# Optimization experiments

Hardware: AMD Instinct MI355X
Metric: run time of the kernel (lower is better)

## Reference

```python
import jax, jax.numpy as jnp
import numpy as np

B, S, D = 4, 2048, 768
H = 12
HD = D // H  # 64

def setup_inputs() -> dict:
    key = jax.random.key(0)
    ks = jax.random.split(key, 5)
    scale = 0.02
    return {
        "x": jax.random.normal(ks[0], (B, S, D), dtype=jnp.float32),
        "w_qkv": jax.random.normal(ks[1], (D, 3 * D), dtype=jnp.float32) * scale,
        "b_qkv": jax.random.normal(ks[2], (3 * D,), dtype=jnp.float32) * scale,
        "w_proj": jax.random.normal(ks[3], (D, D), dtype=jnp.float32) * scale,
        "b_proj": jax.random.normal(ks[4], (D,), dtype=jnp.float32) * scale,
    }

def reference(x, w_qkv, b_qkv, w_proj, b_proj):
    bsz, seq_len, dim = x.shape
    qkv = x @ w_qkv + b_qkv                      # [B,S,3D]
    q, k, v = jnp.split(qkv, 3, axis=-1)
    # [B,S,D] -> [B,H,S,HD]
    def heads(t):
        return t.reshape(bsz, seq_len, H, HD).transpose(0, 2, 1, 3)
    q, k, v = heads(q), heads(k), heads(v)
    scores = jnp.einsum('bhqd,bhkd->bhqk', q, k) * (1.0 / np.sqrt(HD))
    causal = jnp.tril(jnp.ones((seq_len, seq_len), dtype=bool))
    scores = jnp.where(causal[None, None], scores, -jnp.inf)
    attn = jax.nn.softmax(scores.astype(jnp.float32), axis=-1).astype(scores.dtype)
    y = jnp.einsum('bhqk,bhkd->bhqd', attn, v)   # [B,H,S,HD]
    y = y.transpose(0, 2, 1, 3).reshape(bsz, seq_len, dim)
    return y @ w_proj + b_proj
```

## Files before the change

### kernel.cpp

```cpp
#include <hip/hip_runtime.h>
#include <hip/hip_bf16.h>
#include <cstdint>

#define BDIM 768
#define HN 12
#define HDIM 64
#define SEQ 2048
#define BATCH 4
#define MTOT (BATCH * SEQ)

typedef __attribute__((ext_vector_type(8))) short bfrag;
typedef __attribute__((ext_vector_type(4))) float f32x4;

union pfu { bfrag f; unsigned u[4]; };

static __device__ __forceinline__ unsigned short f2bf(float f) {
    union { float f; unsigned u; } v; v.f = f;
    unsigned r = v.u + 0x7FFF + ((v.u >> 16) & 1);
    return (unsigned short)(r >> 16);
}

static __device__ __forceinline__ float fexp2(float x) {
    float r; asm("v_exp_f32 %0, %1" : "=v"(r) : "v"(x)); return r;
}

static __device__ __forceinline__ unsigned cvt_pk_bf16(float lo, float hi) {
    unsigned r;
    asm("v_cvt_pk_bf16_f32 %0, %1, %2" : "=v"(r) : "v"(lo), "v"(hi));
    return r;
}

#if __has_builtin(__builtin_amdgcn_permlane32_swap) && __has_builtin(__builtin_amdgcn_permlane16_swap)
#define HAVE_PERMLANE 1
#else
#define HAVE_PERMLANE 0
#endif

static __device__ __forceinline__ float redmax16(float x) {
#if HAVE_PERMLANE
    union { float f; unsigned u; } a; a.f = x;
    auto r = __builtin_amdgcn_permlane16_swap(a.u, a.u, false, false);
    union { unsigned u; float f; } p, q; p.u = r[0]; q.u = r[1];
    return fmaxf(p.f, q.f);
#else
    return fmaxf(x, __shfl_xor(x, 16));
#endif
}

static __device__ __forceinline__ float redmax32(float x) {
#if HAVE_PERMLANE
    union { float f; unsigned u; } a; a.f = x;
    auto r = __builtin_amdgcn_permlane32_swap(a.u, a.u, false, false);
    union { unsigned u; float f; } p, q; p.u = r[0]; q.u = r[1];
    return fmaxf(p.f, q.f);
#else
    return fmaxf(x, __shfl_xor(x, 32));
#endif
}

__global__ __launch_bounds__(256) void conv_f32_bf16(
    const float* __restrict__ in, unsigned short* __restrict__ out, int n8,
    int* __restrict__ qctr)
{
    if (blockIdx.x == 0 && threadIdx.x < 8) qctr[threadIdx.x] = 0;
    const int i = blockIdx.x * 256 + threadIdx.x;
    if (i >= n8) return;
    const float4 a = ((const float4*)in)[i * 2];
    const float4 b = ((const float4*)in)[i * 2 + 1];
    bfrag o;
    o[0] = f2bf(a.x); o[1] = f2bf(a.y); o[2] = f2bf(a.z); o[3] = f2bf(a.w);
    o[4] = f2bf(b.x); o[5] = f2bf(b.y); o[6] = f2bf(b.z); o[7] = f2bf(b.w);
    ((bfrag*)out)[i] = o;
}

__global__ __launch_bounds__(256) void transpose_f32_bf16(
    const float* __restrict__ in, unsigned short* __restrict__ out, int R, int C)
{
    __shared__ unsigned short t[64][72];
    const int tid = threadIdx.x;
    const int c0 = blockIdx.x * 64, r0 = blockIdx.y * 64;
    #pragma unroll
    for (int i = 0; i < 4; ++i) {
        const int r = (tid >> 4) + i * 16;
        const int c = (tid & 15) * 4;
        const float4 v = *(const float4*)&in[(size_t)(r0 + r) * C + c0 + c];
        t[c + 0][r] = f2bf(v.x);
        t[c + 1][r] = f2bf(v.y);
        t[c + 2][r] = f2bf(v.z);
        t[c + 3][r] = f2bf(v.w);
    }
    __syncthreads();
    #pragma unroll
    for (int i = 0; i < 2; ++i) {
        const int c = (tid >> 3) + i * 32;
        const int r = (tid & 7) * 8;
        *(bfrag*)&out[(size_t)(c0 + c) * R + r0 + r] = *(const bfrag*)&t[c][r];
    }
}

__global__ __launch_bounds__(256) void gemm_qkv(
    const unsigned short* __restrict__ A,
    const unsigned short* __restrict__ Bt,
    const float* __restrict__ bias,
    unsigned short* __restrict__ qb,
    unsigned short* __restrict__ kb,
    unsigned short* __restrict__ vTt)
{
    __shared__ unsigned short As[128 * 64];
    __shared__ unsigned short Bs[128 * 64];

    const int tid  = threadIdx.x;
    const int lane = tid & 63;
    const int wid  = tid >> 6;
    const int l15  = lane & 15;
    const int l4   = lane >> 4;

    const int nwg  = (int)(gridDim.x * gridDim.y);
    const int flat = (int)(blockIdx.y * gridDim.x + blockIdx.x);
    const int swz  = (flat & 7) * (nwg >> 3) + (flat >> 3);
    const int m0 = (swz / (int)gridDim.x) * 128;
    const int n0 = (swz % (int)gridDim.x) * 128;

    const int wm = (wid >> 1) * 64;
    const int wn = (wid & 1) * 64;

    f32x4 acc[4][4] = {};

    for (int k0 = 0; k0 < BDIM; k0 += 64) {
        __syncthreads();
        #pragma unroll
        for (int i = 0; i < 4; ++i) {
            const int row = wid * 32 + i * 8 + (lane >> 3);
            const int ck  = (((lane & 7) ^ (row & 7)) * 8);
            __builtin_amdgcn_global_load_lds(
                (const __attribute__((address_space(1))) void*)(A + (size_t)(m0 + row) * BDIM + k0 + ck),
                (__attribute__((address_space(3))) void*)(As + (wid * 4 + i) * 512),
                16, 0, 0);
            __builtin_amdgcn_global_load_lds(
                (const __attribute__((address_space(1))) void*)(Bt + (size_t)(n0 + row) * BDIM + k0 + ck),
                (__attribute__((address_space(3))) void*)(Bs + (wid * 4 + i) * 512),
                16, 0, 0);
        }
        __syncthreads();

        #pragma unroll
        for (int ks = 0; ks < 2; ++ks) {
            bfrag af[4], bfv[4];
            #pragma unroll
            for (int mi = 0; mi < 4; ++mi) {
                const int row = wm + mi * 16 + l15;
                const int ch  = (ks * 4 + l4) ^ (row & 7);
                af[mi] = *(const bfrag*)(As + row * 64 + ch * 8);
            }
            #pragma unroll
            for (int ni = 0; ni < 4; ++ni) {
                const int row = wn + ni * 16 + l15;
                const int ch  = (ks * 4 + l4) ^ (row & 7);
                bfv[ni] = *(const bfrag*)(Bs + row * 64 + ch * 8);
            }
            #pragma unroll
            for (int mi = 0; mi < 4; ++mi)
                #pragma unroll
                for (int ni = 0; ni < 4; ++ni)
                    acc[mi][ni] = __builtin_amdgcn_mfma_f32_16x16x32_bf16(
                        af[mi], bfv[ni], acc[mi][ni], 0, 0, 0);
        }
    }

    const int nb = n0 + wn;
    if (nb < 1536) {
        unsigned short* dst = (nb < 768) ? qb : kb;
        const int coff = (nb < 768) ? 0 : 768;
        #pragma unroll
        for (int mi = 0; mi < 4; ++mi)
            #pragma unroll
            for (int ni = 0; ni < 4; ++ni) {
                const int n = nb + ni * 16 + l15;
                const float bv = bias[n];
                #pragma unroll
                for (int r = 0; r < 4; ++r) {
                    const int m = m0 + wm + mi * 16 + l4 * 4 + r;
                    dst[(size_t)m * BDIM + (n - coff)] = f2bf(acc[mi][ni][r] + bv);
                }
            }
    } else {
        #pragma unroll
        for (int mi = 0; mi < 4; ++mi)
            #pragma unroll
            for (int ni = 0; ni < 4; ++ni) {
                const int n = nb + ni * 16 + l15;
                const float bv = bias[n];
                const size_t vrow = (size_t)(m0 >> 11) * 768 + (n - 1536);
                const int mbase = m0 + wm + mi * 16 + l4 * 4;
                const int scol = mbase & (SEQ - 1);
                uint2 u2;
                u2.x = (unsigned)f2bf(acc[mi][ni][0] + bv)
                     | ((unsigned)f2bf(acc[mi][ni][1] + bv) << 16);
                u2.y = (unsigned)f2bf(acc[mi][ni][2] + bv)
                     | ((unsigned)f2bf(acc[mi][ni][3] + bv) << 16);
                *(uint2*)(vTt + vrow * SEQ + scol) = u2;
            }
    }
}

__global__ __launch_bounds__(256) void gemm_proj(
    const unsigned short* __restrict__ A,
    const unsigned short* __restrict__ Bt,
    const float* __restrict__ bias,
    float* __restrict__ C)
{
    __shared__ unsigned short As[64 * 64];
    __shared__ unsigned short Bs[128 * 64];

    const int tid  = threadIdx.x;
    const int lane = tid & 63;
    const int wid  = tid >> 6;
    const int l15  = lane & 15;
    const int l4   = lane >> 4;

    const int nwg  = (int)(gridDim.x * gridDim.y);
    const int flat = (int)(blockIdx.y * gridDim.x + blockIdx.x);
    const int swz  = (flat & 7) * (nwg >> 3) + (flat >> 3);
    const int m0 = (swz / (int)gridDim.x) * 64;
    const int n0 = (swz % (int)gridDim.x) * 128;

    const int wm = (wid >> 1) * 32;
    const int wn = (wid & 1) * 64;

    f32x4 acc[2][4] = {};

    for (int k0 = 0; k0 < BDIM; k0 += 64) {
        __syncthreads();
        #pragma unroll
        for (int i = 0; i < 2; ++i) {
            const int row = wid * 16 + i * 8 + (lane >> 3);
            const int ck  = (((lane & 7) ^ (row & 7)) * 8);
            __builtin_amdgcn_global_load_lds(
                (const __attribute__((address_space(1))) void*)(A + (size_t)(m0 + row) * BDIM + k0 + ck),
                (__attribute__((address_space(3))) void*)(As + (wid * 16 + i * 8) * 64),
                16, 0, 0);
        }
        #pragma unroll
        for (int i = 0; i < 4; ++i) {
            const int row = wid * 32 + i * 8 + (lane >> 3);
            const int ck  = (((lane & 7) ^ (row & 7)) * 8);
            __builtin_amdgcn_global_load_lds(
                (const __attribute__((address_space(1))) void*)(Bt + (size_t)(n0 + row) * BDIM + k0 + ck),
                (__attribute__((address_space(3))) void*)(Bs + (wid * 32 + i * 8) * 64),
                16, 0, 0);
        }
        __syncthreads();

        #pragma unroll
        for (int ks = 0; ks < 2; ++ks) {
            bfrag af[2], bfv[4];
            #pragma unroll
            for (int mi = 0; mi < 2; ++mi) {
                const int row = wm + mi * 16 + l15;
                const int ch  = (ks * 4 + l4) ^ (row & 7);
                af[mi] = *(const bfrag*)(As + row * 64 + ch * 8);
            }
            #pragma unroll
            for (int ni = 0; ni < 4; ++ni) {
                const int row = wn + ni * 16 + l15;
                const int ch  = (ks * 4 + l4) ^ (row & 7);
                bfv[ni] = *(const bfrag*)(Bs + row * 64 + ch * 8);
            }
            #pragma unroll
            for (int mi = 0; mi < 2; ++mi)
                #pragma unroll
                for (int ni = 0; ni < 4; ++ni)
                    acc[mi][ni] = __builtin_amdgcn_mfma_f32_16x16x32_bf16(
                        af[mi], bfv[ni], acc[mi][ni], 0, 0, 0);
        }
    }

    #pragma unroll
    for (int mi = 0; mi < 2; ++mi)
        #pragma unroll
        for (int ni = 0; ni < 4; ++ni) {
            const int n = n0 + wn + ni * 16 + l15;
            const float bv = bias[n];
            #pragma unroll
            for (int r = 0; r < 4; ++r) {
                const int m = m0 + wm + mi * 16 + l4 * 4 + r;
                C[(size_t)m * BDIM + n] = acc[mi][ni][r] + bv;
            }
        }
}

#define C2 0.18033688011112042f
#define THR 8.0f

__global__ __launch_bounds__(256, 2) void attn_flash_mfma(
    const unsigned short* __restrict__ qb,
    const unsigned short* __restrict__ kb,
    const unsigned short* __restrict__ vT,
    unsigned short* __restrict__ yatt,
    int* __restrict__ qctr)
{
    __shared__ unsigned short Ks[3][64 * 64];
    __shared__ unsigned short Vs[3][64 * 64];

    const int hint = blockIdx.x & 7;
    const int tid  = threadIdx.x;
    const int lane = tid & 63;
    const int wid  = tid >> 6;
    const int l15  = lane & 15;
    const int l4   = lane >> 4;

    bfrag onesf;
    #pragma unroll
    for (int j = 0; j < 8; ++j) onesf[j] = (short)0x3F80;

    for (;;) {
        __syncthreads();
        if (tid == 0) *(int*)&Ks[0][0] = atomicAdd(&qctr[hint], 1);
        __syncthreads();
        const int it = *(const int*)&Ks[0][0];
        if (it >= 96) break;
        __syncthreads();

        const int bh = hint * 6 + (it % 6);
        const int p  = 15 - (it / 6);
        const int h = bh % HN, b = bh / HN;
        const int q0 = p * 128;
        const int ktmax = 2 * p + 1;

        const unsigned short* kg = kb + (size_t)b * SEQ * BDIM + h * HDIM;
        const unsigned short* vg = vT + (size_t)bh * HDIM * SEQ;

        bfrag qf[2][2];
        {
            const unsigned short* qr0 =
                qb + (size_t)(b * SEQ + q0 + wid * 16 + l15) * BDIM + h * HDIM;
            qf[0][0] = *(const bfrag*)(qr0 + l4 * 8);
            qf[0][1] = *(const bfrag*)(qr0 + 32 + l4 * 8);
            const unsigned short* qr1 = qr0 + (size_t)64 * BDIM;
            qf[1][0] = *(const bfrag*)(qr1 + l4 * 8);
            qf[1][1] = *(const bfrag*)(qr1 + 32 + l4 * 8);
        }

        f32x4 acc0[4] = {}, acc1[4] = {};
        f32x4 accl0 = {}, accl1 = {};
        float m0v = -3.0e38f, m1v = -3.0e38f;

        pfu pf0[2], pf1[2];
        bfrag vr[2][4];
        #pragma unroll
        for (int ks = 0; ks < 2; ++ks) {
            #pragma unroll
            for (int i = 0; i < 4; ++i) { pf0[ks].u[i] = 0u; pf1[ks].u[i] = 0u; }
            #pragma unroll
            for (int ds = 0; ds < 4; ++ds)
                #pragma unroll
                for (int j = 0; j < 8; ++j) vr[ks][ds][j] = 0;
        }

        auto stage = [&](int bufi, int ktile) {
            const int k0 = ktile * 64;
            #pragma unroll
            for (int i = 0; i < 2; ++i) {
                const int row = wid * 16 + i * 8 + (lane >> 3);
                const int ck  = ((lane & 7) ^ (row & 7)) * 8;
                __builtin_amdgcn_global_load_lds(
                    (const __attribute__((address_space(1))) void*)(kg + (size_t)(k0 + row) * BDIM + ck),
                    (__attribute__((address_space(3))) void*)(&Ks[bufi][(wid * 16 + i * 8) * 64]),
                    16, 0, 0);
                __builtin_amdgcn_global_load_lds(
                    (const __attribute__((address_space(1))) void*)(vg + (size_t)row * SEQ + k0 + ck),
                    (__attribute__((address_space(3))) void*)(&Vs[bufi][(wid * 16 + i * 8) * 64]),
                    16, 0, 0);
            }
        };

        auto softmax_dance = [&](f32x4* s, float& mm, pfu* pf, f32x4* acc, f32x4& accl) {
            float mx = s[0][0];
            #pragma unroll
            for (int cs = 0; cs < 4; ++cs)
                #pragma unroll
                for (int r = 0; r < 4; ++r) mx = fmaxf(mx, s[cs][r]);
            mx = redmax16(mx);
            mx = redmax32(mx);
            const float mx2 = mx * C2;

            if (!__all(mx2 <= mm + THR)) {
                const float mnew = fmaxf(mm, mx2);
                const float fac  = fexp2(mm - mnew);
                mm = mnew;
                #pragma unroll
                for (int r = 0; r < 4; ++r) {
                    const float fr = __shfl(fac, (lane & 48) | (l4 * 4 + r));
                    #pragma unroll
                    for (int ds = 0; ds < 4; ++ds) acc[ds][r] *= fr;
                    accl[r] *= fr;
                }
            }

            #pragma unroll
            for (int cs = 0; cs < 4; ++cs)
                #pragma unroll
                for (int r = 0; r < 4; ++r)
                    s[cs][r] = fexp2(fmaf(s[cs][r], C2, -mm));

            unsigned pk[4][2];
            #pragma unroll
            for (int cs = 0; cs < 4; ++cs) {
                pk[cs][0] = cvt_pk_bf16(s[cs][0], s[cs][1]);
                pk[cs][1] = cvt_pk_bf16(s[cs][2], s[cs][3]);
            }
            #pragma unroll
            for (int ks = 0; ks < 2; ++ks)
                #pragma unroll
                for (int i = 0; i < 2; ++i) {
#if HAVE_PERMLANE
                    auto r1 = __builtin_amdgcn_permlane32_swap(
                        pk[ks * 2][i], pk[ks * 2 + 1][i], false, false);
                    auto r2 = __builtin_amdgcn_permlane16_swap(r1[0], r1[1], false, false);
                    pf[ks].u[i]     = r2[0];
                    pf[ks].u[2 + i] = r2[1];
#else
                    const unsigned A  = pk[ks * 2][i];
                    const unsigned B  = pk[ks * 2 + 1][i];
                    const unsigned Ax = __shfl_xor(A, 32);
                    const unsigned Bx = __shfl_xor(B, 32);
                    const unsigned P1 = (l4 < 2) ? A : Bx;
                    const unsigned P2 = (l4 < 2) ? Ax : B;
                    const unsigned S1 = __shfl_xor(P1, 16);
                    const unsigned S2 = __shfl_xor(P2, 16);
                    pf[ks].u[i]     = (l4 & 1) ? S2 : P1;
                    pf[ks].u[2 + i] = (l4 & 1) ? P2 : S1;
#endif
                }
        };

        stage(0, 0);
        stage(1, 1);
        asm volatile("s_waitcnt vmcnt(4) lgkmcnt(0)\ns_barrier" ::: "memory");

        int kt = 0;
        for (;;) {
            const int cb = kt % 3;
            const bool willstage = (kt + 2 <= ktmax);
            if (willstage) stage((kt + 2) % 3, kt + 2);

            const unsigned short* Kb = Ks[cb];
            const unsigned short* Vb = Vs[cb];

            f32x4 s0[4] = {}, s1[4] = {};
            __builtin_amdgcn_s_setprio(1);
            #pragma unroll
            for (int ks = 0; ks < 2; ++ks) {
                #pragma unroll
                for (int cs = 0; cs < 4; ++cs) {
                    const int row = cs * 16 + l15;
                    const int ch  = (ks * 4 + l4) ^ (row & 7);
                    const bfrag kf = *(const bfrag*)(Kb + row * 64 + ch * 8);
                    s0[cs] = __builtin_amdgcn_mfma_f32_16x16x32_bf16(kf, qf[0][ks], s0[cs], 0, 0, 0);
                    s1[cs] = __builtin_amdgcn_mfma_f32_16x16x32_bf16(kf, qf[1][ks], s1[cs], 0, 0, 0);
                }
            }
            #pragma unroll
            for (int ks = 0; ks < 2; ++ks) {
                #pragma unroll
                for (int ds = 0; ds < 4; ++ds) {
                    acc0[ds] = __builtin_amdgcn_mfma_f32_16x16x32_bf16(pf0[ks].f, vr[ks][ds], acc0[ds], 0, 0, 0);
                    acc1[ds] = __builtin_amdgcn_mfma_f32_16x16x32_bf16(pf1[ks].f, vr[ks][ds], acc1[ds], 0, 0, 0);
                }
                accl0 = __builtin_amdgcn_mfma_f32_16x16x32_bf16(pf0[ks].f, onesf, accl0, 0, 0, 0);
                accl1 = __builtin_amdgcn_mfma_f32_16x16x32_bf16(pf1[ks].f, onesf, accl1, 0, 0, 0);
            }
            __builtin_amdgcn_s_setprio(0);

            #pragma unroll
            for (int ks = 0; ks < 2; ++ks)
                #pragma unroll
                for (int ds = 0; ds < 4; ++ds) {
                    const int vrow = ds * 16 + l15;
                    const int vch  = (ks * 4 + l4) ^ (vrow & 7);
                    vr[ks][ds] = *(const bfrag*)(Vb + vrow * 64 + vch * 8);
                }

            if (kt >= 2 * p) {
                const int qg = q0 + wid * 16 + l15;
                #pragma unroll
                for (int cs = 0; cs < 4; ++cs)
                    #pragma unroll
                    for (int r = 0; r < 4; ++r) {
                        const int kgl = kt * 64 + cs * 16 + l4 * 4 + r;
                        if (kgl > qg)      s0[cs][r] = -3.0e38f;
                        if (kgl > qg + 64) s1[cs][r] = -3.0e38f;
                    }
            }

            softmax_dance(s0, m0v, pf0, acc0, accl0);
            softmax_dance(s1, m1v, pf1, acc1, accl1);

            if (kt == ktmax) break;
            if (willstage) {
                asm volatile("s_waitcnt vmcnt(4) lgkmcnt(0)\ns_barrier" ::: "memory");
            } else {
                asm volatile("s_waitcnt vmcnt(0) lgkmcnt(0)\ns_barrier" ::: "memory");
            }
            ++kt;
        }

        #pragma unroll
        for (int ks = 0; ks < 2; ++ks) {
            #pragma unroll
            for (int ds = 0; ds < 4; ++ds) {
                acc0[ds] = __builtin_amdgcn_mfma_f32_16x16x32_bf16(pf0[ks].f, vr[ks][ds], acc0[ds], 0, 0, 0);
                acc1[ds] = __builtin_amdgcn_mfma_f32_16x16x32_bf16(pf1[ks].f, vr[ks][ds], acc1[ds], 0, 0, 0);
            }
            accl0 = __builtin_amdgcn_mfma_f32_16x16x32_bf16(pf0[ks].f, onesf, accl0, 0, 0, 0);
            accl1 = __builtin_amdgcn_mfma_f32_16x16x32_bf16(pf1[ks].f, onesf, accl1, 0, 0, 0);
        }

        #pragma unroll
        for (int r = 0; r < 4; ++r) {
            const float iv0 = 1.f / accl0[r];
            const float iv1 = 1.f / accl1[r];
            unsigned short* o0 =
                yatt + (size_t)(b * SEQ + q0 + wid * 16 + l4 * 4 + r) * BDIM + h * HDIM;
            unsigned short* o1 = o0 + (size_t)64 * BDIM;
            #pragma unroll
            for (int ds = 0; ds < 4; ++ds) {
                o0[ds * 16 + l15] = f2bf(acc0[ds][r] * iv0);
                o1[ds * 16 + l15] = f2bf(acc1[ds][r] * iv1);
            }
        }
    }
}

extern "C" void kernel_launch(void* const* d_in, const int* in_sizes, int n_in,
                              void* d_out, int out_size, void* d_ws, size_t ws_size,
                              hipStream_t stream)
{
    const float* x      = (const float*)d_in[0];
    const float* w_qkv  = (const float*)d_in[1];
    const float* b_qkv  = (const float*)d_in[2];
    const float* w_proj = (const float*)d_in[3];
    const float* b_proj = (const float*)d_in[4];
    float* out = (float*)d_out;

    unsigned short* xb   = (unsigned short*)d_ws;
    unsigned short* qb   = xb  + (size_t)MTOT * BDIM;
    unsigned short* kbuf = qb  + (size_t)MTOT * BDIM;
    unsigned short* vT   = kbuf + (size_t)MTOT * BDIM;
    unsigned short* yatt = vT  + (size_t)MTOT * BDIM;
    unsigned short* wqT  = yatt + (size_t)MTOT * BDIM;
    unsigned short* wpT  = wqT + (size_t)3 * BDIM * BDIM;
    int*            qctr = (int*)(wpT + (size_t)BDIM * BDIM);

    conv_f32_bf16<<<(MTOT * BDIM / 8 + 255) / 256, 256, 0, stream>>>(
        x, xb, MTOT * BDIM / 8, qctr);
    transpose_f32_bf16<<<dim3(3 * BDIM / 64, BDIM / 64), 256, 0, stream>>>(
        w_qkv, wqT, BDIM, 3 * BDIM);
    transpose_f32_bf16<<<dim3(BDIM / 64, BDIM / 64), 256, 0, stream>>>(
        w_proj, wpT, BDIM, BDIM);

    gemm_qkv<<<dim3(3 * BDIM / 128, MTOT / 128), 256, 0, stream>>>(
        xb, wqT, b_qkv, qb, kbuf, vT);

    attn_flash_mfma<<<dim3(512), 256, 0, stream>>>(qb, kbuf, vT, yatt, qctr);

    gemm_proj<<<dim3(BDIM / 128, MTOT / 64), 256, 0, stream>>>(
        yatt, wpT, b_proj, out);
}
```

Before: 137.6 us.

## Enlarge attention query tile to 256 rows per work item

Each persistent-queue work item now covers 256 query rows (four 64-row sub-tiles per block) instead of 128. Every staged K/V tile is therefore reused across twice as many query rows, which halves K/V global-to-LDS traffic and barriers per unit of output. The cost is much higher register pressure (16 accumulator tiles plus 16 score tiles per wave), which can reduce occupancy or cause spills. There are also half as many work items, so load balancing across CUs is coarser.

```diff
diff --git a/kernel.cpp b/kernel.cpp
--- a/kernel.cpp
+++ b/kernel.cpp
@@ -318,44 +318,45 @@
         if (tid == 0) *(int*)&Ks[0][0] = atomicAdd(&qctr[hint], 1);
         __syncthreads();
         const int it = *(const int*)&Ks[0][0];
-        if (it >= 96) break;
+        if (it >= 48) break;
         __syncthreads();
 
         const int bh = hint * 6 + (it % 6);
-        const int p  = 15 - (it / 6);
+        const int p  = 7 - (it / 6);
         const int h = bh % HN, b = bh / HN;
-        const int q0 = p * 128;
-        const int ktmax = 2 * p + 1;
+        const int q0 = p * 256;
+        const int ktmax = 4 * p + 3;
 
         const unsigned short* kg = kb + (size_t)b * SEQ * BDIM + h * HDIM;
         const unsigned short* vg = vT + (size_t)bh * HDIM * SEQ;
 
-        bfrag qf[2][2];
-        {
-            const unsigned short* qr0 =
-                qb + (size_t)(b * SEQ + q0 + wid * 16 + l15) * BDIM + h * HDIM;
-            qf[0][0] = *(const bfrag*)(qr0 + l4 * 8);
-            qf[0][1] = *(const bfrag*)(qr0 + 32 + l4 * 8);
-            const unsigned short* qr1 = qr0 + (size_t)64 * BDIM;
-            qf[1][0] = *(const bfrag*)(qr1 + l4 * 8);
-            qf[1][1] = *(const bfrag*)(qr1 + 32 + l4 * 8);
-        }
-
-        f32x4 acc0[4] = {}, acc1[4] = {};
-        f32x4 accl0 = {}, accl1 = {};
-        float m0v = -3.0e38f, m1v = -3.0e38f;
-
-        pfu pf0[2], pf1[2];
+        bfrag qf[4][2];
+        #pragma unroll
+        for (int s = 0; s < 4; ++s) {
+            const unsigned short* qr =
+                qb + (size_t)(b * SEQ + q0 + s * 64 + wid * 16 + l15) * BDIM + h * HDIM;
+            qf[s][0] = *(const bfrag*)(qr + l4 * 8);
+            qf[s][1] = *(const bfrag*)(qr + 32 + l4 * 8);
+        }
+
+        f32x4 acc[4][4] = {};
+        f32x4 accl[4]   = {};
+        float mrow[4] = {-3.0e38f, -3.0e38f, -3.0e38f, -3.0e38f};
+
+        pfu pf[4][2];
         bfrag vr[2][4];
         #pragma unroll
-        for (int ks = 0; ks < 2; ++ks) {
-            #pragma unroll
-            for (int i = 0; i < 4; ++i) { pf0[ks].u[i] = 0u; pf1[ks].u[i] = 0u; }
+        for (int s = 0; s < 4; ++s)
+            #pragma unroll
+            for (int ks = 0; ks < 2; ++ks)
+                #pragma unroll
+                for (int i = 0; i < 4; ++i) pf[s][ks].u[i] = 0u;
+        #pragma unroll
+        for (int ks = 0; ks < 2; ++ks)
             #pragma unroll
             for (int ds = 0; ds < 4; ++ds)
                 #pragma unroll
                 for (int j = 0; j < 8; ++j) vr[ks][ds][j] = 0;
-        }
 
         auto stage = [&](int bufi, int ktile) {
             const int k0 = ktile * 64;
@@ -374,7 +375,7 @@
             }
         };
 
-        auto softmax_dance = [&](f32x4* s, float& mm, pfu* pf, f32x4* acc, f32x4& accl) {
+        auto softmax_dance = [&](f32x4* s, float& mm, pfu* pfs, f32x4* ac, f32x4& acl) {
             float mx = s[0][0];
             #pragma unroll
             for (int cs = 0; cs < 4; ++cs)
@@ -392,8 +393,8 @@
                 for (int r = 0; r < 4; ++r) {
                     const float fr = __shfl(fac, (lane & 48) | (l4 * 4 + r));
                     #pragma unroll
-                    for (int ds = 0; ds < 4; ++ds) acc[ds][r] *= fr;
-                    accl[r] *= fr;
+                    for (int ds = 0; ds < 4; ++ds) ac[ds][r] *= fr;
+                    acl[r] *= fr;
                 }
             }
 
@@ -417,8 +418,8 @@
                     auto r1 = __builtin_amdgcn_permlane32_swap(
                         pk[ks * 2][i], pk[ks * 2 + 1][i], false, false);
                     auto r2 = __builtin_amdgcn_permlane16_swap(r1[0], r1[1], false, false);
-                    pf[ks].u[i]     = r2[0];
-                    pf[ks].u[2 + i] = r2[1];
+                    pfs[ks].u[i]     = r2[0];
+                    pfs[ks].u[2 + i] = r2[1];
 #else
                     const unsigned A  = pk[ks * 2][i];
                     const unsigned B  = pk[ks * 2 + 1][i];
@@ -428,8 +429,8 @@
                     const unsigned P2 = (l4 < 2) ? Ax : B;
                     const unsigned S1 = __shfl_xor(P1, 16);
                     const unsigned S2 = __shfl_xor(P2, 16);
-                    pf[ks].u[i]     = (l4 & 1) ? S2 : P1;
-                    pf[ks].u[2 + i] = (l4 & 1) ? P2 : S1;
+                    pfs[ks].u[i]     = (l4 & 1) ? S2 : P1;
+                    pfs[ks].u[2 + i] = (l4 & 1) ? P2 : S1;
 #endif
                 }
         };
@@ -447,7 +448,12 @@
             const unsigned short* Kb = Ks[cb];
             const unsigned short* Vb = Vs[cb];
 
-            f32x4 s0[4] = {}, s1[4] = {};
+            f32x4 st[4][4];
+            #pragma unroll
+            for (int s = 0; s < 4; ++s)
+                #pragma unroll
+                for (int cs = 0; cs < 4; ++cs) st[s][cs] = f32x4{};
+
             __builtin_amdgcn_s_setprio(1);
             #pragma unroll
             for (int ks = 0; ks < 2; ++ks) {
@@ -456,19 +462,24 @@
                     const int row = cs * 16 + l15;
                     const int ch  = (ks * 4 + l4) ^ (row & 7);
                     const bfrag kf = *(const bfrag*)(Kb + row * 64 + ch * 8);
-                    s0[cs] = __builtin_amdgcn_mfma_f32_16x16x32_bf16(kf, qf[0][ks], s0[cs], 0, 0, 0);
-                    s1[cs] = __builtin_amdgcn_mfma_f32_16x16x32_bf16(kf, qf[1][ks], s1[cs], 0, 0, 0);
+                    #pragma unroll
+                    for (int s = 0; s < 4; ++s)
+                        st[s][cs] = __builtin_amdgcn_mfma_f32_16x16x32_bf16(
+                            kf, qf[s][ks], st[s][cs], 0, 0, 0);
                 }
             }
             #pragma unroll
             for (int ks = 0; ks < 2; ++ks) {
                 #pragma unroll
-                for (int ds = 0; ds < 4; ++ds) {
-                    acc0[ds] = __builtin_amdgcn_mfma_f32_16x16x32_bf16(pf0[ks].f, vr[ks][ds], acc0[ds], 0, 0, 0);
-                    acc1[ds] = __builtin_amdgcn_mfma_f32_16x16x32_bf16(pf1[ks].f, vr[ks][ds], acc1[ds], 0, 0, 0);
-                }
-                accl0 = __builtin_amdgcn_mfma_f32_16x16x32_bf16(pf0[ks].f, onesf, accl0, 0, 0, 0);
-                accl1 = __builtin_amdgcn_mfma_f32_16x16x32_bf16(pf1[ks].f, onesf, accl1, 0, 0, 0);
+                for (int ds = 0; ds < 4; ++ds)
+                    #pragma unroll
+                    for (int s = 0; s < 4; ++s)
+                        acc[s][ds] = __builtin_amdgcn_mfma_f32_16x16x32_bf16(
+                            pf[s][ks].f, vr[ks][ds], acc[s][ds], 0, 0, 0);
+                #pragma unroll
+                for (int s = 0; s < 4; ++s)
+                    accl[s] = __builtin_amdgcn_mfma_f32_16x16x32_bf16(
+                        pf[s][ks].f, onesf, accl[s], 0, 0, 0);
             }
             __builtin_amdgcn_s_setprio(0);
 
@@ -481,20 +492,22 @@
                     vr[ks][ds] = *(const bfrag*)(Vb + vrow * 64 + vch * 8);
                 }
 
-            if (kt >= 2 * p) {
+            if (kt >= 4 * p) {
                 const int qg = q0 + wid * 16 + l15;
                 #pragma unroll
                 for (int cs = 0; cs < 4; ++cs)
                     #pragma unroll
                     for (int r = 0; r < 4; ++r) {
                         const int kgl = kt * 64 + cs * 16 + l4 * 4 + r;
-                        if (kgl > qg)      s0[cs][r] = -3.0e38f;
-                        if (kgl > qg + 64) s1[cs][r] = -3.0e38f;
+                        #pragma unroll
+                        for (int s = 0; s < 4; ++s)
+                            if (kgl > qg + s * 64) st[s][cs][r] = -3.0e38f;
                     }
             }
 
-            softmax_dance(s0, m0v, pf0, acc0, accl0);
-            softmax_dance(s1, m1v, pf1, acc1, accl1);
+            #pragma unroll
+            for (int s = 0; s < 4; ++s)
+                softmax_dance(st[s], mrow[s], pf[s], acc[s], accl[s]);
 
             if (kt == ktmax) break;
             if (willstage) {
@@ -508,25 +521,28 @@
         #pragma unroll
         for (int ks = 0; ks < 2; ++ks) {
             #pragma unroll
-            for (int ds = 0; ds < 4; ++ds) {
-                acc0[ds] = __builtin_amdgcn_mfma_f32_16x16x32_bf16(pf0[ks].f, vr[ks][ds], acc0[ds], 0, 0, 0);
-                acc1[ds] = __builtin_amdgcn_mfma_f32_16x16x32_bf16(pf1[ks].f, vr[ks][ds], acc1[ds], 0, 0, 0);
-            }
-            accl0 = __builtin_amdgcn_mfma_f32_16x16x32_bf16(pf0[ks].f, onesf, accl0, 0, 0, 0);
-            accl1 = __builtin_amdgcn_mfma_f32_16x16x32_bf16(pf1[ks].f, onesf, accl1, 0, 0, 0);
-        }
-
-        #pragma unroll
-        for (int r = 0; r < 4; ++r) {
-            const float iv0 = 1.f / accl0[r];
-            const float iv1 = 1.f / accl1[r];
-            unsigned short* o0 =
-                yatt + (size_t)(b * SEQ + q0 + wid * 16 + l4 * 4 + r) * BDIM + h * HDIM;
-            unsigned short* o1 = o0 + (size_t)64 * BDIM;
-            #pragma unroll
-            for (int ds = 0; ds < 4; ++ds) {
-                o0[ds * 16 + l15] = f2bf(acc0[ds][r] * iv0);
-                o1[ds * 16 + l15] = f2bf(acc1[ds][r] * iv1);
+            for (int ds = 0; ds < 4; ++ds)
+                #pragma unroll
+                for (int s = 0; s < 4; ++s)
+                    acc[s][ds] = __builtin_amdgcn_mfma_f32_16x16x32_bf16(
+                        pf[s][ks].f, vr[ks][ds], acc[s][ds], 0, 0, 0);
+            #pragma unroll
+            for (int s = 0; s < 4; ++s)
+                accl[s] = __builtin_amdgcn_mfma_f32_16x16x32_bf16(
+                    pf[s][ks].f, onesf, accl[s], 0, 0, 0);
+        }
+
+        #pragma unroll
+        for (int s = 0; s < 4; ++s) {
+            #pragma unroll
+            for (int r = 0; r < 4; ++r) {
+                const float iv = 1.f / accl[s][r];
+                unsigned short* o =
+                    yatt + (size_t)(b * SEQ + q0 + s * 64 + wid * 16 + l4 * 4 + r) * BDIM
+                    + h * HDIM;
+                #pragma unroll
+                for (int ds = 0; ds < 4; ++ds)
+                    o[ds * 16 + l15] = f2bf(acc[s][ds][r] * iv);
             }
         }
     }
```

After: 237.4 us. 72.6% more time.
